# Optimization experiments

Hardware: AMD Instinct MI355X
Metric: run time of the kernel (lower is better)

Reference implementation:

```python
import jax, jax.numpy as jnp
import numpy as np

N = 100000
F_IN = 128
HID = 128
NCLS = 40
NEG_SLOPE = 0.2
BN_EPS = 1e-5


def setup_inputs() -> dict:
    key = jax.random.key(0)
    ks = jax.random.split(key, 16)
    x = jax.random.normal(ks[0], (N, F_IN), dtype=jnp.float32)
    # self-loop-free random edges: dst = (src + 1 + r) % N
    E = 1600000
    src = jax.random.randint(ks[1], (E,), 0, N)
    off = jax.random.randint(ks[2], (E,), 1, N)
    dst = (src + off) % N
    edge_index = jnp.stack([src, dst]).astype(jnp.int64)

    def glorot(k, shape):
        fan = shape[0] + shape[-1]
        s = jnp.sqrt(6.0 / fan)
        return jax.random.uniform(k, shape, jnp.float32, -s, s)

    params = {
        'W1': glorot(ks[3], (F_IN, HID)),
        'as1': glorot(ks[4], (HID,)), 'ad1': glorot(ks[5], (HID,)),
        'b1': jnp.zeros((HID,), jnp.float32),
        'g1': jnp.ones((HID,), jnp.float32), 'beta1': jnp.zeros((HID,), jnp.float32),
        'W2': glorot(ks[6], (HID, HID)),
        'as2': glorot(ks[7], (HID,)), 'ad2': glorot(ks[8], (HID,)),
        'b2': jnp.zeros((HID,), jnp.float32),
        'g2': jnp.ones((HID,), jnp.float32), 'beta2': jnp.zeros((HID,), jnp.float32),
        'Wc': glorot(ks[9], (HID, NCLS)),
        'bc': jnp.zeros((NCLS,), jnp.float32),
    }
    return {'x': x, 'edge_index': edge_index, **params}


def _gat_conv(h_in, src, dst, W, a_src, a_dst, bias):
    # heads=1, concat=False -> single head, mean over heads is identity
    h = h_in @ W                               # [N, C]
    alpha_s = h @ a_src                        # [N]
    alpha_d = h @ a_dst                        # [N]
    alpha = alpha_s[src] + alpha_d[dst]        # [E] edge score
    alpha = jax.nn.leaky_relu(alpha, NEG_SLOPE)
    # segment softmax over destination node neighborhoods
    m = jax.ops.segment_max(alpha, dst, num_segments=N)
    e = jnp.exp(alpha - m[dst])
    s = jax.ops.segment_sum(e, dst, num_segments=N)
    alpha = e / s[dst]
    msg = h[src] * alpha[:, None]              # [E, C]
    out = jax.ops.segment_sum(msg, dst, num_segments=N)
    return out + bias


def _batchnorm(x, gamma, beta):
    mu = jnp.mean(x, axis=0)
    var = jnp.mean(jnp.square(x - mu), axis=0)  # biased, as torch BN training
    return (x - mu) * jax.lax.rsqrt(var + BN_EPS) * gamma + beta


def reference(x, edge_index, W1, as1, ad1, b1, g1, beta1,
              W2, as2, ad2, b2, g2, beta2, Wc, bc):
    src, dst = edge_index[0], edge_index[1]
    # add self loops (input edges are guaranteed self-loop-free)
    loop = jnp.arange(N, dtype=src.dtype)
    src = jnp.concatenate([src, loop])
    dst = jnp.concatenate([dst, loop])

    h = _gat_conv(x, src, dst, W1, as1, ad1, b1)
    h = jax.nn.relu(_batchnorm(h, g1, beta1))
    h = _gat_conv(h, src, dst, W2, as2, ad2, b2)
    h = jax.nn.relu(_batchnorm(h, g2, beta2))
    return h @ Wc + bc
```

## Files before the change

kernel.cpp:

```cpp
#include <hip/hip_runtime.h>
#include <hip/hip_fp16.h>
#include <math.h>


#define CDIM 128
#define NCLS_ 40
#define NEG_SLOPE_ 0.2f
#define BN_EPS_ 1e-5f
#define BRNG 256
#define BCAP 6144
#define EPB 16

using short8  = __attribute__((ext_vector_type(8))) short;
using short4v = __attribute__((ext_vector_type(4))) short;
using f32x4   = __attribute__((ext_vector_type(4))) float;

static __device__ __forceinline__ float lrelu(float a) {
    return a > 0.f ? a : NEG_SLOPE_ * a;
}
static __device__ __forceinline__ short f2bf(float f) {
    unsigned u = __float_as_uint(f);
    u += 0x7fffu + ((u >> 16) & 1u);
    return (short)(u >> 16);
}
static __device__ __forceinline__ float bf_lo(unsigned u) { return __uint_as_float(u << 16); }
static __device__ __forceinline__ float bf_hi(unsigned u) { return __uint_as_float(u & 0xffff0000u); }
static __device__ __forceinline__ __half2 u2h2(unsigned u) { return __builtin_bit_cast(__half2, u); }
static __device__ __forceinline__ unsigned h22u(__half2 h) { return __builtin_bit_cast(unsigned, h); }

__global__ void k_setup(int* bcur, float* bnsum, int NB, int n, int E, int* offs,
                        const float* __restrict__ W1, const float* __restrict__ W2,
                        const float* __restrict__ Wc,
                        short* __restrict__ Wt1, short* __restrict__ Wt2,
                        short* __restrict__ Wtc) {
    int i = blockIdx.x * blockDim.x + threadIdx.x;
    if (i < NB) bcur[i] = 0;
    if (i < 512) bnsum[i] = 0.f;
    if (i == 0) offs[n] = E + n;
    if (i < 128 * 128) {
        int k = i >> 7, nn = i & 127;
        Wt1[nn * 128 + k] = f2bf(W1[i]);
        Wt2[nn * 128 + k] = f2bf(W2[i]);
    }
    if (i < 48 * 128) {
        int nn = i >> 7, k = i & 127;
        Wtc[i] = (nn < NCLS_) ? f2bf(Wc[k * NCLS_ + nn]) : (short)0;
    }
}

__global__ __launch_bounds__(256) void k_binA(
    const int* __restrict__ src, const int* __restrict__ dst, int E,
    int* __restrict__ bcur, uint2* __restrict__ bucket, int NB)
{
    __shared__ int hist[400];
    __shared__ int base[400];
    int t = threadIdx.x;
    long e0 = (long)blockIdx.x * (256 * EPB) + t;

    for (int i = t; i < NB; i += 256) hist[i] = 0;
    __syncthreads();

    int sv[EPB], dv[EPB];
    #pragma unroll
    for (int i = 0; i < EPB; i++) {
        long e = e0 + (long)i * 256;
        if (e < E) {
            sv[i] = src[e]; dv[i] = dst[e];
            atomicAdd(&hist[dv[i] >> 8], 1);
        } else dv[i] = -1;
    }
    __syncthreads();

    for (int i = t; i < NB; i += 256) {
        int h = hist[i];
        base[i] = (h > 0) ? atomicAdd(&bcur[i], h) : 0;
    }
    __syncthreads();
    for (int i = t; i < NB; i += 256) hist[i] = 0;
    __syncthreads();

    #pragma unroll
    for (int i = 0; i < EPB; i++) {
        if (dv[i] >= 0) {
            int b = dv[i] >> 8;
            int pos = base[b] + atomicAdd(&hist[b], 1);
            if (pos < BCAP)
                bucket[(size_t)b * BCAP + pos] =
                    make_uint2((unsigned)sv[i], (unsigned)dv[i]);
        }
    }
}

__global__ __launch_bounds__(256) void k_fillB(
    const uint2* __restrict__ bucket, const int* __restrict__ bcur,
    int n, int NB, int* __restrict__ offs, int* __restrict__ csr)
{
    __shared__ int hist[256];
    __shared__ int scanb[256];
    __shared__ int cur[256];
    __shared__ int buf[BCAP + BRNG];
    int b = blockIdx.x, t = threadIdx.x;
    int node0 = b << 8;
    int nodesIn = min(BRNG, n - node0);
    int cnt = min(bcur[b], BCAP);
    const uint2* mybkt = bucket + (size_t)b * BCAP;

    int part = 0;
    for (int j = t; j < b; j += 256) part += min(bcur[j], BCAP);
    scanb[t] = part; __syncthreads();
    for (int s2 = 128; s2 > 0; s2 >>= 1) {
        if (t < s2) scanb[t] += scanb[t + s2];
        __syncthreads();
    }
    int base = scanb[0] + node0;
    __syncthreads();

    hist[t] = 0; __syncthreads();
    for (int e2 = t; e2 < cnt; e2 += 256)
        atomicAdd(&hist[mybkt[e2].y & 255], 1);
    __syncthreads();

    int v = hist[t] + ((t < nodesIn) ? 1 : 0);
    scanb[t] = v; __syncthreads();
    for (int d = 1; d < 256; d <<= 1) {
        int x2 = (t >= d) ? scanb[t - d] : 0;
        __syncthreads();
        scanb[t] += x2;
        __syncthreads();
    }
    int lo = scanb[t] - v;
    if (t < nodesIn) {
        offs[node0 + t] = base + lo;
        buf[lo] = node0 + t;
        cur[t] = lo + 1;
    }
    __syncthreads();

    for (int e2 = t; e2 < cnt; e2 += 256) {
        uint2 ed = mybkt[e2];
        int pos = atomicAdd(&cur[ed.y & 255], 1);
        buf[pos] = (int)ed.x;
    }
    __syncthreads();

    int tot = cnt + nodesIn;
    for (int j2 = t; j2 < tot; j2 += 256) csr[base + j2] = buf[j2];
}

__global__ __launch_bounds__(256) void k_gemm_mfma(
    const float* __restrict__ Xf, const unsigned* __restrict__ Xb,
    const short* __restrict__ Wt,
    const float* __restrict__ bnsum, const float* __restrict__ gamma,
    const float* __restrict__ beta, float invn,
    const float* __restrict__ av_s, const float* __restrict__ av_d,
    short* __restrict__ Hh, float* __restrict__ alpha_s, float* __restrict__ alpha_d,
    int n, int fuse)
{
    __shared__ short As[64 * 128];
    __shared__ short Bs[128 * 128];
    __shared__ float part_s[4][64];
    __shared__ float part_d[4][64];
    int t = threadIdx.x;
    int row0 = blockIdx.x * 64;

    for (int j = 0; j < 8; j++) {
        int idx = j * 256 + t;
        int nn = idx >> 4, cc = idx & 15;
        *(short8*)(Bs + nn * 128 + cc * 8) = *(const short8*)(Wt + nn * 128 + cc * 8);
    }
    float4 sc4 = make_float4(1.f, 1.f, 1.f, 1.f);
    float4 sh4 = make_float4(0.f, 0.f, 0.f, 0.f);
    if (fuse) {
        int cb = (t & 31) * 4;
        float4 s0 = *(const float4*)(bnsum + cb);
        float4 s1 = *(const float4*)(bnsum + 128 + cb);
        float4 gm = *(const float4*)(gamma + cb);
        float4 bt = *(const float4*)(beta + cb);
        float mean, var;
        mean = s0.x * invn; var = fmaxf(s1.x * invn - mean * mean, 0.f);
        sc4.x = gm.x * rsqrtf(var + BN_EPS_); sh4.x = bt.x - mean * sc4.x;
        mean = s0.y * invn; var = fmaxf(s1.y * invn - mean * mean, 0.f);
        sc4.y = gm.y * rsqrtf(var + BN_EPS_); sh4.y = bt.y - mean * sc4.y;
        mean = s0.z * invn; var = fmaxf(s1.z * invn - mean * mean, 0.f);
        sc4.z = gm.z * rsqrtf(var + BN_EPS_); sh4.z = bt.z - mean * sc4.z;
        mean = s0.w * invn; var = fmaxf(s1.w * invn - mean * mean, 0.f);
        sc4.w = gm.w * rsqrtf(var + BN_EPS_); sh4.w = bt.w - mean * sc4.w;
    }
    for (int j = 0; j < 8; j++) {
        int idx = j * 256 + t;
        int r = idx >> 5, k4 = idx & 31;
        int gr = row0 + r;
        float4 xv = make_float4(0.f, 0.f, 0.f, 0.f);
        if (fuse) {
            if (gr < n) {
                uint2 u = *(const uint2*)(Xb + (size_t)gr * 64 + k4 * 2);
                xv.x = bf_lo(u.x); xv.y = bf_hi(u.x);
                xv.z = bf_lo(u.y); xv.w = bf_hi(u.y);
            }
            xv.x = fmaxf(fmaf(xv.x, sc4.x, sh4.x), 0.f);
            xv.y = fmaxf(fmaf(xv.y, sc4.y, sh4.y), 0.f);
            xv.z = fmaxf(fmaf(xv.z, sc4.z, sh4.z), 0.f);
            xv.w = fmaxf(fmaf(xv.w, sc4.w, sh4.w), 0.f);
        } else {
            if (gr < n) xv = *(const float4*)(Xf + (size_t)gr * CDIM + k4 * 4);
        }
        short4v o;
        o.x = f2bf(xv.x); o.y = f2bf(xv.y); o.z = f2bf(xv.z); o.w = f2bf(xv.w);
        *(short4v*)(As + r * 128 + k4 * 4) = o;
    }
    __syncthreads();

    int w = t >> 6, lane = t & 63, q = lane >> 4, c = lane & 15;
    f32x4 zero = {0.f, 0.f, 0.f, 0.f};
    f32x4 acc[4][2];
    for (int i = 0; i < 4; i++) { acc[i][0] = zero; acc[i][1] = zero; }

    for (int ks = 0; ks < 4; ks++) {
        int k0 = ks * 32 + q * 8;
        short8 a0 = *(short8*)(As + (c) * 128 + k0);
        short8 a1 = *(short8*)(As + (16 + c) * 128 + k0);
        short8 a2 = *(short8*)(As + (32 + c) * 128 + k0);
        short8 a3 = *(short8*)(As + (48 + c) * 128 + k0);
        short8 b0 = *(short8*)(Bs + (w * 32 + c) * 128 + k0);
        short8 b1 = *(short8*)(Bs + (w * 32 + 16 + c) * 128 + k0);
        acc[0][0] = __builtin_amdgcn_mfma_f32_16x16x32_bf16(a0, b0, acc[0][0], 0, 0, 0);
        acc[1][0] = __builtin_amdgcn_mfma_f32_16x16x32_bf16(a1, b0, acc[1][0], 0, 0, 0);
        acc[2][0] = __builtin_amdgcn_mfma_f32_16x16x32_bf16(a2, b0, acc[2][0], 0, 0, 0);
        acc[3][0] = __builtin_amdgcn_mfma_f32_16x16x32_bf16(a3, b0, acc[3][0], 0, 0, 0);
        acc[0][1] = __builtin_amdgcn_mfma_f32_16x16x32_bf16(a0, b1, acc[0][1], 0, 0, 0);
        acc[1][1] = __builtin_amdgcn_mfma_f32_16x16x32_bf16(a1, b1, acc[1][1], 0, 0, 0);
        acc[2][1] = __builtin_amdgcn_mfma_f32_16x16x32_bf16(a2, b1, acc[2][1], 0, 0, 0);
        acc[3][1] = __builtin_amdgcn_mfma_f32_16x16x32_bf16(a3, b1, acc[3][1], 0, 0, 0);
    }

    float as0 = av_s[w * 32 + c],      as1 = av_s[w * 32 + 16 + c];
    float ad0 = av_d[w * 32 + c],      ad1 = av_d[w * 32 + 16 + c];
    #pragma unroll
    for (int mt = 0; mt < 4; mt++) {
        #pragma unroll
        for (int r = 0; r < 4; r++) {
            float v0 = acc[mt][0][r], v1 = acc[mt][1][r];
            float ps = v0 * as0 + v1 * as1;
            float pd = v0 * ad0 + v1 * ad1;
            #pragma unroll
            for (int off = 1; off < 16; off <<= 1) {
                ps += __shfl_xor(ps, off);
                pd += __shfl_xor(pd, off);
            }
            if (c == 0) {
                part_s[w][mt * 16 + q * 4 + r] = ps;
                part_d[w][mt * 16 + q * 4 + r] = pd;
            }
        }
    }
    __syncthreads();

    short* Hs = As;
    #pragma unroll
    for (int mt = 0; mt < 4; mt++)
        #pragma unroll
        for (int nt = 0; nt < 2; nt++)
            #pragma unroll
            for (int r = 0; r < 4; r++)
                Hs[(mt * 16 + q * 4 + r) * 128 + w * 32 + nt * 16 + c] =
                    (short)__half_as_ushort(__float2half_rn(acc[mt][nt][r]));

    if (t < 64) {
        int row = row0 + t;
        if (row < n) {
            alpha_s[row] = part_s[0][t] + part_s[1][t] + part_s[2][t] + part_s[3][t];
            alpha_d[row] = part_d[0][t] + part_d[1][t] + part_d[2][t] + part_d[3][t];
        }
    }
    __syncthreads();

    for (int j = 0; j < 4; j++) {
        int idx = j * 256 + t;
        int r = idx >> 4, cc = idx & 15;
        int gr = row0 + r;
        if (gr < n)
            *(short8*)(Hh + (size_t)gr * 128 + cc * 8) = *(short8*)(Hs + r * 128 + cc * 8);
    }
}

__global__ __launch_bounds__(256) void k_agg(
    const unsigned* __restrict__ Hh, const int* __restrict__ offs,
    const int* __restrict__ csr, const float* __restrict__ alpha_s,
    const float* __restrict__ alpha_d, const float* __restrict__ bias,
    unsigned* __restrict__ Ob, int n)
{
    int i = blockIdx.x * 4 + (threadIdx.x >> 6);
    int lane = threadIdx.x & 63;
    if (i >= n) return;
    int o0 = offs[i], o1 = offs[i + 1];
    float adi = alpha_d[i];

    float m = -1e30f;
    float se = 0.f;
    __half2 acc2 = __floats2half2_rn(0.f, 0.f);

    for (int c0 = o0; c0 < o1; c0 += 64) {
        int j = c0 + lane;
        int cnt = min(64, o1 - c0);
        int sj = (j < o1) ? csr[j] : 0;

        unsigned ua[8], ub[8], uc[8];
        #pragma unroll
        for (int q = 0; q < 8; q++) {
            int s = __builtin_amdgcn_readlane(sj, q);
            ua[q] = Hh[(size_t)(unsigned)s * 64 + lane];
        }
        if (cnt > 8) {
            #pragma unroll
            for (int q = 0; q < 8; q++) {
                int s = __builtin_amdgcn_readlane(sj, 8 + q);
                ub[q] = Hh[(size_t)(unsigned)s * 64 + lane];
            }
        }
        if (cnt > 16) {
            #pragma unroll
            for (int q = 0; q < 8; q++) {
                int s = __builtin_amdgcn_readlane(sj, 16 + q);
                uc[q] = Hh[(size_t)(unsigned)s * 64 + lane];
            }
        }

        float a = (j < o1) ? lrelu(alpha_s[sj] + adi) : -1e30f;
        float cm = a;
        #pragma unroll
        for (int o = 32; o > 0; o >>= 1) cm = fmaxf(cm, __shfl_xor(cm, o));
        if (cm > m) {
            float r = __expf(m - cm);
            se *= r;
            acc2 = __hmul2(acc2, __float2half2_rn(r));
            m = cm;
        }
        float wl = (j < o1) ? __expf(a - m) : 0.f;
        se += wl;
        int wli = (int)h22u(__float2half2_rn(wl));

        for (int b = 0; b < cnt; b += 24) {
            #pragma unroll
            for (int q = 0; q < 8; q++) {
                int wq = __builtin_amdgcn_readlane(wli, b + q);
                acc2 = __hfma2(u2h2(ua[q]), u2h2((unsigned)wq), acc2);
            }
            if (b + 24 < cnt) {
                #pragma unroll
                for (int q = 0; q < 8; q++) {
                    int s = __builtin_amdgcn_readlane(sj, b + 24 + q);
                    ua[q] = Hh[(size_t)(unsigned)s * 64 + lane];
                }
            }
            if (b + 8 < cnt) {
                #pragma unroll
                for (int q = 0; q < 8; q++) {
                    int wq = __builtin_amdgcn_readlane(wli, b + 8 + q);
                    acc2 = __hfma2(u2h2(ub[q]), u2h2((unsigned)wq), acc2);
                }
                if (b + 32 < cnt) {
                    #pragma unroll
                    for (int q = 0; q < 8; q++) {
                        int s = __builtin_amdgcn_readlane(sj, b + 32 + q);
                        ub[q] = Hh[(size_t)(unsigned)s * 64 + lane];
                    }
                }
                if (b + 16 < cnt) {
                    #pragma unroll
                    for (int q = 0; q < 8; q++) {
                        int wq = __builtin_amdgcn_readlane(wli, b + 16 + q);
                        acc2 = __hfma2(u2h2(uc[q]), u2h2((unsigned)wq), acc2);
                    }
                    if (b + 40 < cnt) {
                        #pragma unroll
                        for (int q = 0; q < 8; q++) {
                            int s = __builtin_amdgcn_readlane(sj, b + 40 + q);
                            uc[q] = Hh[(size_t)(unsigned)s * 64 + lane];
                        }
                    }
                }
            }
        }
    }

    #pragma unroll
    for (int o = 32; o > 0; o >>= 1) se += __shfl_xor(se, o);
    float inv = 1.f / se;
    float2 af = __half22float2(acc2);
    float2 b2 = *(const float2*)(bias + lane * 2);
    float rx = fmaf(af.x, inv, b2.x);
    float ry = fmaf(af.y, inv, b2.y);
    unsigned pack = ((unsigned)(unsigned short)f2bf(ry) << 16) |
                    (unsigned)(unsigned short)f2bf(rx);
    Ob[(size_t)i * 64 + lane] = pack;
}

__global__ void k_bnstats(const unsigned* __restrict__ Hb, int n, float* __restrict__ sums) {
    __shared__ float red[4][64][4];
    int w = threadIdx.x & 63;
    int g = threadIdx.x >> 6;
    float slo = 0.f, shi = 0.f, qlo = 0.f, qhi = 0.f;
    for (int r = blockIdx.x * 4 + g; r < n; r += gridDim.x * 4) {
        unsigned u = Hb[(size_t)r * 64 + w];
        float lo = bf_lo(u), hi = bf_hi(u);
        slo += lo; shi += hi; qlo += lo * lo; qhi += hi * hi;
    }
    red[g][w][0] = slo; red[g][w][1] = shi; red[g][w][2] = qlo; red[g][w][3] = qhi;
    __syncthreads();
    if (threadIdx.x < 64) {
        int w2 = threadIdx.x;
        float s0 = 0.f, s1 = 0.f, s2 = 0.f, s3 = 0.f;
        for (int gg = 0; gg < 4; gg++) {
            s0 += red[gg][w2][0]; s1 += red[gg][w2][1];
            s2 += red[gg][w2][2]; s3 += red[gg][w2][3];
        }
        atomicAdd(&sums[2 * w2], s0);
        atomicAdd(&sums[2 * w2 + 1], s1);
        atomicAdd(&sums[128 + 2 * w2], s2);
        atomicAdd(&sums[128 + 2 * w2 + 1], s3);
    }
}

__global__ __launch_bounds__(256) void k_cls(
    const unsigned* __restrict__ G, const short* __restrict__ Wtc,
    const float* __restrict__ bc, const float* __restrict__ bnsum,
    const float* __restrict__ gamma, const float* __restrict__ beta, float invn,
    float* __restrict__ out, int n)
{
    __shared__ short As[64 * 128];
    __shared__ short Bs[48 * 128];
    int t = threadIdx.x;
    int row0 = blockIdx.x * 64;

    for (int j = 0; j < 3; j++) {
        int idx = j * 256 + t;
        *(short8*)(Bs + idx * 8) = *(const short8*)(Wtc + idx * 8);
    }
    float4 sc4, sh4;
    {
        int cb = (t & 31) * 4;
        float4 s0 = *(const float4*)(bnsum + cb);
        float4 s1 = *(const float4*)(bnsum + 128 + cb);
        float4 gm = *(const float4*)(gamma + cb);
        float4 bt = *(const float4*)(beta + cb);
        float mean, var;
        mean = s0.x * invn; var = fmaxf(s1.x * invn - mean * mean, 0.f);
        sc4.x = gm.x * rsqrtf(var + BN_EPS_); sh4.x = bt.x - mean * sc4.x;
        mean = s0.y * invn; var = fmaxf(s1.y * invn - mean * mean, 0.f);
        sc4.y = gm.y * rsqrtf(var + BN_EPS_); sh4.y = bt.y - mean * sc4.y;
        mean = s0.z * invn; var = fmaxf(s1.z * invn - mean * mean, 0.f);
        sc4.z = gm.z * rsqrtf(var + BN_EPS_); sh4.z = bt.z - mean * sc4.z;
        mean = s0.w * invn; var = fmaxf(s1.w * invn - mean * mean, 0.f);
        sc4.w = gm.w * rsqrtf(var + BN_EPS_); sh4.w = bt.w - mean * sc4.w;
    }
    for (int j = 0; j < 8; j++) {
        int idx = j * 256 + t;
        int r = idx >> 5, k4 = idx & 31;
        int gr = row0 + r;
        float4 xv = make_float4(0.f, 0.f, 0.f, 0.f);
        if (gr < n) {
            uint2 u = *(const uint2*)(G + (size_t)gr * 64 + k4 * 2);
            xv.x = bf_lo(u.x); xv.y = bf_hi(u.x);
            xv.z = bf_lo(u.y); xv.w = bf_hi(u.y);
        }
        xv.x = fmaxf(fmaf(xv.x, sc4.x, sh4.x), 0.f);
        xv.y = fmaxf(fmaf(xv.y, sc4.y, sh4.y), 0.f);
        xv.z = fmaxf(fmaf(xv.z, sc4.z, sh4.z), 0.f);
        xv.w = fmaxf(fmaf(xv.w, sc4.w, sh4.w), 0.f);
        short4v o;
        o.x = f2bf(xv.x); o.y = f2bf(xv.y); o.z = f2bf(xv.z); o.w = f2bf(xv.w);
        *(short4v*)(As + r * 128 + k4 * 4) = o;
    }
    __syncthreads();

    int w = t >> 6, lane = t & 63, q = lane >> 4, c = lane & 15;
    f32x4 zero = {0.f, 0.f, 0.f, 0.f};
    f32x4 acc[3] = {zero, zero, zero};
    for (int ks = 0; ks < 4; ks++) {
        int k0 = ks * 32 + q * 8;
        short8 a  = *(short8*)(As + (w * 16 + c) * 128 + k0);
        short8 b0 = *(short8*)(Bs + (c) * 128 + k0);
        short8 b1 = *(short8*)(Bs + (16 + c) * 128 + k0);
        short8 b2 = *(short8*)(Bs + (32 + c) * 128 + k0);
        acc[0] = __builtin_amdgcn_mfma_f32_16x16x32_bf16(a, b0, acc[0], 0, 0, 0);
        acc[1] = __builtin_amdgcn_mfma_f32_16x16x32_bf16(a, b1, acc[1], 0, 0, 0);
        acc[2] = __builtin_amdgcn_mfma_f32_16x16x32_bf16(a, b2, acc[2], 0, 0, 0);
    }
    float bc0 = bc[c], bc1 = bc[16 + c], bc2 = (c < 8) ? bc[32 + c] : 0.f;
    #pragma unroll
    for (int r = 0; r < 4; r++) {
        int row = row0 + w * 16 + q * 4 + r;
        if (row < n) {
            out[(size_t)row * NCLS_ + c]      = acc[0][r] + bc0;
            out[(size_t)row * NCLS_ + 16 + c] = acc[1][r] + bc1;
            if (c < 8) out[(size_t)row * NCLS_ + 32 + c] = acc[2][r] + bc2;
        }
    }
}

extern "C" void kernel_launch(void* const* d_in, const int* in_sizes, int n_in,
                              void* d_out, int out_size, void* d_ws, size_t ws_size,
                              hipStream_t stream)
{
    const float* x   = (const float*)d_in[0];
    const int*   ei  = (const int*)d_in[1];
    const float* W1  = (const float*)d_in[2];
    const float* as1 = (const float*)d_in[3];
    const float* ad1 = (const float*)d_in[4];
    const float* b1  = (const float*)d_in[5];
    const float* g1  = (const float*)d_in[6];
    const float* be1 = (const float*)d_in[7];
    const float* W2  = (const float*)d_in[8];
    const float* as2 = (const float*)d_in[9];
    const float* ad2 = (const float*)d_in[10];
    const float* b2  = (const float*)d_in[11];
    const float* g2  = (const float*)d_in[12];
    const float* be2 = (const float*)d_in[13];
    const float* Wc  = (const float*)d_in[14];
    const float* bc  = (const float*)d_in[15];
    float* out = (float*)d_out;

    int n = in_sizes[0] / CDIM;
    int E = in_sizes[1] / 2;
    const int* src = ei;
    const int* dst = ei + E;
    float invn = 1.f / (float)n;
    int NB = (n + BRNG - 1) / BRNG;

    char* p = (char*)d_ws;
    auto alloc = [&p](size_t bytes) { char* q = p; p += (bytes + 63) & ~(size_t)63; return q; };
    short*    Hh      = (short*)alloc((size_t)n * CDIM * sizeof(short));
    unsigned* bufB    = (unsigned*)alloc((size_t)n * 64 * sizeof(unsigned));
    float*    alpha_s = (float*)alloc((size_t)n * sizeof(float));
    float*    alpha_d = (float*)alloc((size_t)n * sizeof(float));
    float*    bnsum   = (float*)alloc(512 * sizeof(float));
    short*    Wt1     = (short*)alloc(128 * 128 * sizeof(short));
    short*    Wt2     = (short*)alloc(128 * 128 * sizeof(short));
    short*    Wtc     = (short*)alloc(48 * 128 * sizeof(short));
    int*      bcurs   = (int*)alloc((size_t)NB * sizeof(int));
    int*      offs    = (int*)alloc((size_t)(n + 1) * sizeof(int));
    uint2*    bucket  = (uint2*)alloc((size_t)NB * BCAP * sizeof(uint2));
    int*      csr     = (int*)alloc((size_t)(E + n) * sizeof(int));

    k_setup<<<dim3(64), dim3(256), 0, stream>>>(bcurs, bnsum, NB, n, E, offs,
                                                W1, W2, Wc, Wt1, Wt2, Wtc);
    k_binA<<<dim3((E + 4095) / 4096), dim3(256), 0, stream>>>(src, dst, E, bcurs, bucket, NB);
    k_fillB<<<dim3(NB), dim3(256), 0, stream>>>(bucket, bcurs, n, NB, offs, csr);

    dim3 ggrid((n + 63) / 64);
    dim3 wgrid((n + 3) / 4);

    k_gemm_mfma<<<ggrid, 256, 0, stream>>>(x, nullptr, Wt1, nullptr, nullptr, nullptr,
                                           invn, as1, ad1, Hh, alpha_s, alpha_d, n, 0);
    k_agg<<<wgrid, 256, 0, stream>>>((const unsigned*)Hh, offs, csr, alpha_s, alpha_d,
                                     b1, bufB, n);
    k_bnstats<<<dim3(256), dim3(256), 0, stream>>>(bufB, n, bnsum);

    k_gemm_mfma<<<ggrid, 256, 0, stream>>>(nullptr, bufB, Wt2, bnsum, g1, be1,
                                           invn, as2, ad2, Hh, alpha_s, alpha_d, n, 1);
    k_agg<<<wgrid, 256, 0, stream>>>((const unsigned*)Hh, offs, csr, alpha_s, alpha_d,
                                     b2, bufB, n);
    k_bnstats<<<dim3(256), dim3(256), 0, stream>>>(bufB, n, bnsum + 256);

    k_cls<<<ggrid, 256, 0, stream>>>(bufB, Wtc, bc, bnsum + 256, g2, be2, invn, out, n);
}
```

Baseline: 436.0 us.

## Split GAT aggregation into softmax-weight pass and packed gather pass

```diff
diff --git a/kernel.cpp b/kernel.cpp
--- a/kernel.cpp
+++ b/kernel.cpp
@@ -26,7 +26,6 @@
 static __device__ __forceinline__ float bf_lo(unsigned u) { return __uint_as_float(u << 16); }
 static __device__ __forceinline__ float bf_hi(unsigned u) { return __uint_as_float(u & 0xffff0000u); }
 static __device__ __forceinline__ __half2 u2h2(unsigned u) { return __builtin_bit_cast(__half2, u); }
-static __device__ __forceinline__ unsigned h22u(__half2 h) { return __builtin_bit_cast(unsigned, h); }
 
 __global__ void k_setup(int* bcur, float* bnsum, int NB, int n, int E, int* offs,
                         const float* __restrict__ W1, const float* __restrict__ W2,
@@ -283,99 +282,140 @@
     }
 }
 
-__global__ __launch_bounds__(256) void k_agg(
-    const unsigned* __restrict__ Hh, const int* __restrict__ offs,
-    const int* __restrict__ csr, const float* __restrict__ alpha_s,
-    const float* __restrict__ alpha_d, const float* __restrict__ bias,
-    unsigned* __restrict__ Ob, int n)
+__global__ __launch_bounds__(256) void k_wts(
+    const int* __restrict__ offs, const int* __restrict__ csr,
+    const float* __restrict__ alpha_s, const float* __restrict__ alpha_d,
+    unsigned* __restrict__ pkbuf, float* __restrict__ invb, int n)
 {
     int i = blockIdx.x * 4 + (threadIdx.x >> 6);
     int lane = threadIdx.x & 63;
     if (i >= n) return;
     int o0 = offs[i], o1 = offs[i + 1];
     float adi = alpha_d[i];
-
-    float m = -1e30f;
-    float se = 0.f;
+    int deg = o1 - o0;
+
+    if (deg <= 64) {
+        int j = o0 + lane;
+        bool v = j < o1;
+        int sj = v ? csr[j] : 0;
+        float a = v ? lrelu(alpha_s[sj] + adi) : -1e30f;
+        float m = a;
+        #pragma unroll
+        for (int o = 32; o > 0; o >>= 1) m = fmaxf(m, __shfl_xor(m, o));
+        float e = v ? __expf(a - m) : 0.f;
+        float se = e;
+        #pragma unroll
+        for (int o = 32; o > 0; o >>= 1) se += __shfl_xor(se, o);
+        if (v) {
+            unsigned h = (unsigned)__half_as_ushort(__float2half_rn(e));
+            pkbuf[j] = ((unsigned)sj << 15) | h;
+        }
+        if (lane == 0) invb[i] = 1.f / se;
+    } else {
+        float m = -1e30f;
+        for (int c0 = o0; c0 < o1; c0 += 64) {
+            int j = c0 + lane;
+            float a = (j < o1) ? lrelu(alpha_s[csr[j]] + adi) : -1e30f;
+            m = fmaxf(m, a);
+        }
+        #pragma unroll
+        for (int o = 32; o > 0; o >>= 1) m = fmaxf(m, __shfl_xor(m, o));
+        float se = 0.f;
+        for (int c0 = o0; c0 < o1; c0 += 64) {
+            int j = c0 + lane;
+            if (j < o1) {
+                int sj = csr[j];
+                float a = lrelu(alpha_s[sj] + adi);
+                float e = __expf(a - m);
+                se += e;
+                unsigned h = (unsigned)__half_as_ushort(__float2half_rn(e));
+                pkbuf[j] = ((unsigned)sj << 15) | h;
+            }
+        }
+        #pragma unroll
+        for (int o = 32; o > 0; o >>= 1) se += __shfl_xor(se, o);
+        if (lane == 0) invb[i] = 1.f / se;
+    }
+}
+
+__global__ __launch_bounds__(256) void k_gather(
+    const unsigned* __restrict__ Hh, const int* __restrict__ offs,
+    const unsigned* __restrict__ pkbuf, const float* __restrict__ invb,
+    const float* __restrict__ bias, unsigned* __restrict__ Ob, int n)
+{
+    int i = blockIdx.x * 4 + (threadIdx.x >> 6);
+    int lane = threadIdx.x & 63;
+    if (i >= n) return;
+    int o0 = offs[i], o1 = offs[i + 1];
     __half2 acc2 = __floats2half2_rn(0.f, 0.f);
 
     for (int c0 = o0; c0 < o1; c0 += 64) {
         int j = c0 + lane;
         int cnt = min(64, o1 - c0);
-        int sj = (j < o1) ? csr[j] : 0;
+        int pk = (j < o1) ? (int)pkbuf[j] : 0;
 
         unsigned ua[8], ub[8], uc[8];
+        int pa[8], pb[8], pc[8];
         #pragma unroll
         for (int q = 0; q < 8; q++) {
-            int s = __builtin_amdgcn_readlane(sj, q);
-            ua[q] = Hh[(size_t)(unsigned)s * 64 + lane];
+            pa[q] = __builtin_amdgcn_readlane(pk, q);
+            ua[q] = Hh[(size_t)((unsigned)pa[q] >> 15) * 64 + lane];
         }
         if (cnt > 8) {
             #pragma unroll
             for (int q = 0; q < 8; q++) {
-                int s = __builtin_amdgcn_readlane(sj, 8 + q);
-                ub[q] = Hh[(size_t)(unsigned)s * 64 + lane];
+                pb[q] = __builtin_amdgcn_readlane(pk, 8 + q);
+                ub[q] = Hh[(size_t)((unsigned)pb[q] >> 15) * 64 + lane];
             }
         }
         if (cnt > 16) {
             #pragma unroll
             for (int q = 0; q < 8; q++) {
-                int s = __builtin_amdgcn_readlane(sj, 16 + q);
-                uc[q] = Hh[(size_t)(unsigned)s * 64 + lane];
-            }
-        }
-
-        float a = (j < o1) ? lrelu(alpha_s[sj] + adi) : -1e30f;
-        float cm = a;
-        #pragma unroll
-        for (int o = 32; o > 0; o >>= 1) cm = fmaxf(cm, __shfl_xor(cm, o));
-        if (cm > m) {
-            float r = __expf(m - cm);
-            se *= r;
-            acc2 = __hmul2(acc2, __float2half2_rn(r));
-            m = cm;
-        }
-        float wl = (j < o1) ? __expf(a - m) : 0.f;
-        se += wl;
-        int wli = (int)h22u(__float2half2_rn(wl));
+                pc[q] = __builtin_amdgcn_readlane(pk, 16 + q);
+                uc[q] = Hh[(size_t)((unsigned)pc[q] >> 15) * 64 + lane];
+            }
+        }
 
         for (int b = 0; b < cnt; b += 24) {
             #pragma unroll
             for (int q = 0; q < 8; q++) {
-                int wq = __builtin_amdgcn_readlane(wli, b + q);
-                acc2 = __hfma2(u2h2(ua[q]), u2h2((unsigned)wq), acc2);
+                unsigned hw = (unsigned)pa[q] & 0x7fffu;
+                hw |= hw << 16;
+                acc2 = __hfma2(u2h2(ua[q]), u2h2(hw), acc2);
             }
             if (b + 24 < cnt) {
                 #pragma unroll
                 for (int q = 0; q < 8; q++) {
-                    int s = __builtin_amdgcn_readlane(sj, b + 24 + q);
-                    ua[q] = Hh[(size_t)(unsigned)s * 64 + lane];
+                    pa[q] = __builtin_amdgcn_readlane(pk, b + 24 + q);
+                    ua[q] = Hh[(size_t)((unsigned)pa[q] >> 15) * 64 + lane];
                 }
             }
             if (b + 8 < cnt) {
                 #pragma unroll
                 for (int q = 0; q < 8; q++) {
-                    int wq = __builtin_amdgcn_readlane(wli, b + 8 + q);
-                    acc2 = __hfma2(u2h2(ub[q]), u2h2((unsigned)wq), acc2);
+                    unsigned hw = (unsigned)pb[q] & 0x7fffu;
+                    hw |= hw << 16;
+                    acc2 = __hfma2(u2h2(ub[q]), u2h2(hw), acc2);
                 }
                 if (b + 32 < cnt) {
                     #pragma unroll
                     for (int q = 0; q < 8; q++) {
-                        int s = __builtin_amdgcn_readlane(sj, b + 32 + q);
-                        ub[q] = Hh[(size_t)(unsigned)s * 64 + lane];
+                        pb[q] = __builtin_amdgcn_readlane(pk, b + 32 + q);
+                        ub[q] = Hh[(size_t)((unsigned)pb[q] >> 15) * 64 + lane];
                     }
                 }
                 if (b + 16 < cnt) {
                     #pragma unroll
                     for (int q = 0; q < 8; q++) {
-                        int wq = __builtin_amdgcn_readlane(wli, b + 16 + q);
-                        acc2 = __hfma2(u2h2(uc[q]), u2h2((unsigned)wq), acc2);
+                        unsigned hw = (unsigned)pc[q] & 0x7fffu;
+                        hw |= hw << 16;
+                        acc2 = __hfma2(u2h2(uc[q]), u2h2(hw), acc2);
                     }
                     if (b + 40 < cnt) {
                         #pragma unroll
                         for (int q = 0; q < 8; q++) {
-                            int s = __builtin_amdgcn_readlane(sj, b + 40 + q);
-                            uc[q] = Hh[(size_t)(unsigned)s * 64 + lane];
+                            pc[q] = __builtin_amdgcn_readlane(pk, b + 40 + q);
+                            uc[q] = Hh[(size_t)((unsigned)pc[q] >> 15) * 64 + lane];
                         }
                     }
                 }
@@ -383,9 +423,7 @@
         }
     }
 
-    #pragma unroll
-    for (int o = 32; o > 0; o >>= 1) se += __shfl_xor(se, o);
-    float inv = 1.f / se;
+    float inv = invb[i];
     float2 af = __half22float2(acc2);
     float2 b2 = *(const float2*)(bias + lane * 2);
     float rx = fmaf(af.x, inv, b2.x);
@@ -542,6 +580,9 @@
     uint2*    bucket  = (uint2*)alloc((size_t)NB * BCAP * sizeof(uint2));
     int*      csr     = (int*)alloc((size_t)(E + n) * sizeof(int));
 
+    unsigned* pkbuf = (unsigned*)bucket;
+    float*    invb  = (float*)((char*)bucket + (((size_t)(E + n) * 4 + 63) & ~(size_t)63));
+
     k_setup<<<dim3(64), dim3(256), 0, stream>>>(bcurs, bnsum, NB, n, E, offs,
                                                 W1, W2, Wc, Wt1, Wt2, Wtc);
     k_binA<<<dim3((E + 4095) / 4096), dim3(256), 0, stream>>>(src, dst, E, bcurs, bucket, NB);
@@ -552,14 +593,14 @@
 
     k_gemm_mfma<<<ggrid, 256, 0, stream>>>(x, nullptr, Wt1, nullptr, nullptr, nullptr,
                                            invn, as1, ad1, Hh, alpha_s, alpha_d, n, 0);
-    k_agg<<<wgrid, 256, 0, stream>>>((const unsigned*)Hh, offs, csr, alpha_s, alpha_d,
-                                     b1, bufB, n);
+    k_wts<<<wgrid, 256, 0, stream>>>(offs, csr, alpha_s, alpha_d, pkbuf, invb, n);
+    k_gather<<<wgrid, 256, 0, stream>>>((const unsigned*)Hh, offs, pkbuf, invb, b1, bufB, n);
     k_bnstats<<<dim3(256), dim3(256), 0, stream>>>(bufB, n, bnsum);
 
     k_gemm_mfma<<<ggrid, 256, 0, stream>>>(nullptr, bufB, Wt2, bnsum, g1, be1,
                                            invn, as2, ad2, Hh, alpha_s, alpha_d, n, 1);
-    k_agg<<<wgrid, 256, 0, stream>>>((const unsigned*)Hh, offs, csr, alpha_s, alpha_d,
-                                     b2, bufB, n);
+    k_wts<<<wgrid, 256, 0, stream>>>(offs, csr, alpha_s, alpha_d, pkbuf, invb, n);
+    k_gather<<<wgrid, 256, 0, stream>>>((const unsigned*)Hh, offs, pkbuf, invb, b2, bufB, n);
     k_bnstats<<<dim3(256), dim3(256), 0, stream>>>(bufB, n, bnsum + 256);
 
     k_cls<<<ggrid, 256, 0, stream>>>(bufB, Wtc, bc, bnsum + 256, g2, be2, invn, out, n);
```

New measurement: 480.4 us. 10.2% more time.

## Fold attention vectors into weights and compute alpha scores with an extra MFMA

Applied to the files above, without the earlier changes.

```diff
diff --git a/kernel.cpp b/kernel.cpp
--- a/kernel.cpp
+++ b/kernel.cpp
@@ -31,8 +31,11 @@
 __global__ void k_setup(int* bcur, float* bnsum, int NB, int n, int E, int* offs,
                         const float* __restrict__ W1, const float* __restrict__ W2,
                         const float* __restrict__ Wc,
+                        const float* __restrict__ as1, const float* __restrict__ ad1,
+                        const float* __restrict__ as2, const float* __restrict__ ad2,
                         short* __restrict__ Wt1, short* __restrict__ Wt2,
-                        short* __restrict__ Wtc) {
+                        short* __restrict__ Wtc,
+                        short* __restrict__ wsd1, short* __restrict__ wsd2) {
     int i = blockIdx.x * blockDim.x + threadIdx.x;
     if (i < NB) bcur[i] = 0;
     if (i < 512) bnsum[i] = 0.f;
@@ -45,6 +48,16 @@
     if (i < 48 * 128) {
         int nn = i >> 7, k = i & 127;
         Wtc[i] = (nn < NCLS_) ? f2bf(Wc[k * NCLS_ + nn]) : (short)0;
+    }
+    if (i < 128) {
+        float s1 = 0.f, d1 = 0.f, s2 = 0.f, d2 = 0.f;
+        for (int nn2 = 0; nn2 < 128; nn2++) {
+            float w1v = W1[i * 128 + nn2], w2v = W2[i * 128 + nn2];
+            s1 = fmaf(w1v, as1[nn2], s1); d1 = fmaf(w1v, ad1[nn2], d1);
+            s2 = fmaf(w2v, as2[nn2], s2); d2 = fmaf(w2v, ad2[nn2], d2);
+        }
+        wsd1[i] = f2bf(s1); wsd1[128 + i] = f2bf(d1);
+        wsd2[i] = f2bf(s2); wsd2[128 + i] = f2bf(d2);
     }
 }
 
@@ -149,17 +162,15 @@
 
 __global__ __launch_bounds__(256) void k_gemm_mfma(
     const float* __restrict__ Xf, const unsigned* __restrict__ Xb,
-    const short* __restrict__ Wt,
+    const short* __restrict__ Wt, const short* __restrict__ wsd,
     const float* __restrict__ bnsum, const float* __restrict__ gamma,
     const float* __restrict__ beta, float invn,
-    const float* __restrict__ av_s, const float* __restrict__ av_d,
     short* __restrict__ Hh, float* __restrict__ alpha_s, float* __restrict__ alpha_d,
     int n, int fuse)
 {
     __shared__ short As[64 * 128];
     __shared__ short Bs[128 * 128];
-    __shared__ float part_s[4][64];
-    __shared__ float part_d[4][64];
+    __shared__ short wl[256];
     int t = threadIdx.x;
     int row0 = blockIdx.x * 64;
 
@@ -168,6 +179,7 @@
         int nn = idx >> 4, cc = idx & 15;
         *(short8*)(Bs + nn * 128 + cc * 8) = *(const short8*)(Wt + nn * 128 + cc * 8);
     }
+    if (t < 256) wl[t] = wsd[t];
     float4 sc4 = make_float4(1.f, 1.f, 1.f, 1.f);
     float4 sh4 = make_float4(0.f, 0.f, 0.f, 0.f);
     if (fuse) {
@@ -213,6 +225,7 @@
     int w = t >> 6, lane = t & 63, q = lane >> 4, c = lane & 15;
     f32x4 zero = {0.f, 0.f, 0.f, 0.f};
     f32x4 acc[4][2];
+    f32x4 acc_a = zero;
     for (int i = 0; i < 4; i++) { acc[i][0] = zero; acc[i][1] = zero; }
 
     for (int ks = 0; ks < 4; ks++) {
@@ -231,28 +244,17 @@
         acc[1][1] = __builtin_amdgcn_mfma_f32_16x16x32_bf16(a1, b1, acc[1][1], 0, 0, 0);
         acc[2][1] = __builtin_amdgcn_mfma_f32_16x16x32_bf16(a2, b1, acc[2][1], 0, 0, 0);
         acc[3][1] = __builtin_amdgcn_mfma_f32_16x16x32_bf16(a3, b1, acc[3][1], 0, 0, 0);
-    }
-
-    float as0 = av_s[w * 32 + c],      as1 = av_s[w * 32 + 16 + c];
-    float ad0 = av_d[w * 32 + c],      ad1 = av_d[w * 32 + 16 + c];
-    #pragma unroll
-    for (int mt = 0; mt < 4; mt++) {
+
+        short8 ba;
         #pragma unroll
-        for (int r = 0; r < 4; r++) {
-            float v0 = acc[mt][0][r], v1 = acc[mt][1][r];
-            float ps = v0 * as0 + v1 * as1;
-            float pd = v0 * ad0 + v1 * ad1;
-            #pragma unroll
-            for (int off = 1; off < 16; off <<= 1) {
-                ps += __shfl_xor(ps, off);
-                pd += __shfl_xor(pd, off);
-            }
-            if (c == 0) {
-                part_s[w][mt * 16 + q * 4 + r] = ps;
-                part_d[w][mt * 16 + q * 4 + r] = pd;
-            }
-        }
-    }
+        for (int jj = 0; jj < 8; jj++) {
+            short vs = wl[k0 + jj], vd = wl[128 + k0 + jj];
+            ba[jj] = (c == 0) ? vs : ((c == 1) ? vd : (short)0);
+        }
+        short8 aw = (w == 0) ? a0 : ((w == 1) ? a1 : ((w == 2) ? a2 : a3));
+        acc_a = __builtin_amdgcn_mfma_f32_16x16x32_bf16(aw, ba, acc_a, 0, 0, 0);
+    }
+
     __syncthreads();
 
     short* Hs = As;
@@ -265,11 +267,14 @@
                 Hs[(mt * 16 + q * 4 + r) * 128 + w * 32 + nt * 16 + c] =
                     (short)__half_as_ushort(__float2half_rn(acc[mt][nt][r]));
 
-    if (t < 64) {
-        int row = row0 + t;
-        if (row < n) {
-            alpha_s[row] = part_s[0][t] + part_s[1][t] + part_s[2][t] + part_s[3][t];
-            alpha_d[row] = part_d[0][t] + part_d[1][t] + part_d[2][t] + part_d[3][t];
+    if (c < 2) {
+        #pragma unroll
+        for (int r = 0; r < 4; r++) {
+            int row = row0 + w * 16 + q * 4 + r;
+            if (row < n) {
+                if (c == 0) alpha_s[row] = acc_a[r];
+                else        alpha_d[row] = acc_a[r];
+            }
         }
     }
     __syncthreads();
@@ -335,9 +340,9 @@
             acc2 = __hmul2(acc2, __float2half2_rn(r));
             m = cm;
         }
-        float wl = (j < o1) ? __expf(a - m) : 0.f;
-        se += wl;
-        int wli = (int)h22u(__float2half2_rn(wl));
+        float wl2 = (j < o1) ? __expf(a - m) : 0.f;
+        se += wl2;
+        int wli = (int)h22u(__float2half2_rn(wl2));
 
         for (int b = 0; b < cnt; b += 24) {
             #pragma unroll
@@ -537,27 +542,30 @@
     short*    Wt1     = (short*)alloc(128 * 128 * sizeof(short));
     short*    Wt2     = (short*)alloc(128 * 128 * sizeof(short));
     short*    Wtc     = (short*)alloc(48 * 128 * sizeof(short));
+    short*    wsd1    = (short*)alloc(256 * sizeof(short));
+    short*    wsd2    = (short*)alloc(256 * sizeof(short));
     int*      bcurs   = (int*)alloc((size_t)NB * sizeof(int));
     int*      offs    = (int*)alloc((size_t)(n + 1) * sizeof(int));
     uint2*    bucket  = (uint2*)alloc((size_t)NB * BCAP * sizeof(uint2));
     int*      csr     = (int*)alloc((size_t)(E + n) * sizeof(int));
 
     k_setup<<<dim3(64), dim3(256), 0, stream>>>(bcurs, bnsum, NB, n, E, offs,
-                                                W1, W2, Wc, Wt1, Wt2, Wtc);
+                                                W1, W2, Wc, as1, ad1, as2, ad2,
+                                                Wt1, Wt2, Wtc, wsd1, wsd2);
     k_binA<<<dim3((E + 4095) / 4096), dim3(256), 0, stream>>>(src, dst, E, bcurs, bucket, NB);
     k_fillB<<<dim3(NB), dim3(256), 0, stream>>>(bucket, bcurs, n, NB, offs, csr);
 
     dim3 ggrid((n + 63) / 64);
     dim3 wgrid((n + 3) / 4);
 
-    k_gemm_mfma<<<ggrid, 256, 0, stream>>>(x, nullptr, Wt1, nullptr, nullptr, nullptr,
-                                           invn, as1, ad1, Hh, alpha_s, alpha_d, n, 0);
+    k_gemm_mfma<<<ggrid, 256, 0, stream>>>(x, nullptr, Wt1, wsd1, nullptr, nullptr,
+                                           nullptr, invn, Hh, alpha_s, alpha_d, n, 0);
     k_agg<<<wgrid, 256, 0, stream>>>((const unsigned*)Hh, offs, csr, alpha_s, alpha_d,
                                      b1, bufB, n);
     k_bnstats<<<dim3(256), dim3(256), 0, stream>>>(bufB, n, bnsum);
 
-    k_gemm_mfma<<<ggrid, 256, 0, stream>>>(nullptr, bufB, Wt2, bnsum, g1, be1,
-                                           invn, as2, ad2, Hh, alpha_s, alpha_d, n, 1);
+    k_gemm_mfma<<<ggrid, 256, 0, stream>>>(nullptr, bufB, Wt2, wsd2, bnsum, g1,
+                                           be1, invn, Hh, alpha_s, alpha_d, n, 1);
     k_agg<<<wgrid, 256, 0, stream>>>((const unsigned*)Hh, offs, csr, alpha_s, alpha_d,
                                      b2, bufB, n);
     k_bnstats<<<dim3(256), dim3(256), 0, stream>>>(bufB, n, bnsum + 256);
```

After: 436.1 us. Within noise of the previous version (+0.0%).
